# Kernel optimization log

Hardware: AMD Instinct MI355X
Metric: run time of the kernel (lower is better)

The kernel has to match this reference:

```python
import jax, jax.numpy as jnp
import numpy as np

MODES = 256
WIDTH = 64
T_HIST = 1
T_FUT = 1
BATCH = 64
S = 8192


def setup_inputs() -> dict:
    key = jax.random.key(0)
    ks = jax.random.split(key, 12)
    scale = 1.0 / (WIDTH * WIDTH)
    inp = {
        "u": jax.random.normal(ks[0], (BATCH, S, T_HIST), dtype=jnp.float32),
        # lifting layer: Linear(T_HIST+1 -> WIDTH), stored [in, out]
        "fc0_w": jax.random.normal(ks[1], (T_HIST + 1, WIDTH), dtype=jnp.float32) * 0.5,
        "fc0_b": jax.random.normal(ks[2], (WIDTH,), dtype=jnp.float32) * 0.1,
        # 4 spectral conv layers, complex weights stored as real/imag parts
        "sw_r": scale * jax.random.uniform(ks[3], (4, WIDTH, WIDTH, MODES), dtype=jnp.float32),
        "sw_i": scale * jax.random.uniform(ks[4], (4, WIDTH, WIDTH, MODES), dtype=jnp.float32),
        # 4 pointwise (1x1 conv) layers: weight [out,in], bias [out]
        "pw_w": jax.random.normal(ks[5], (4, WIDTH, WIDTH), dtype=jnp.float32) * (1.0 / np.sqrt(WIDTH)),
        "pw_b": jax.random.normal(ks[6], (4, WIDTH), dtype=jnp.float32) * 0.1,
        # projection head
        "fc1_w": jax.random.normal(ks[7], (WIDTH, 128), dtype=jnp.float32) * (1.0 / np.sqrt(WIDTH)),
        "fc1_b": jax.random.normal(ks[8], (128,), dtype=jnp.float32) * 0.1,
        "fc2_w": jax.random.normal(ks[9], (128, T_FUT), dtype=jnp.float32) * (1.0 / np.sqrt(128)),
        "fc2_b": jax.random.normal(ks[10], (T_FUT,), dtype=jnp.float32) * 0.1,
    }
    return inp


def _spectral_conv(x, wr, wi):
    # x: [b, c_in, s] real; weights: [c_in, c_out, MODES] (real/imag parts)
    s = x.shape[-1]
    xf = jnp.fft.rfft(x)                     # [b, c_in, s//2+1] complex
    w = wr + 1j * wi
    om = jnp.einsum('bix,iox->box', xf[:, :, :MODES], w)  # [b, c_out, MODES]
    out_ft = jnp.zeros((x.shape[0], wr.shape[1], s // 2 + 1), dtype=om.dtype)
    out_ft = out_ft.at[:, :, :MODES].set(om)
    return jnp.fft.irfft(out_ft, n=s)        # [b, c_out, s] real


def reference(u, fc0_w, fc0_b, sw_r, sw_i, pw_w, pw_b, fc1_w, fc1_b, fc2_w, fc2_b):
    b, s, _ = u.shape
    grid = jnp.broadcast_to(jnp.linspace(0.0, 1.0, s, dtype=u.dtype)[None, :, None], (b, s, 1))
    x = jnp.concatenate([u, grid], axis=-1)              # [b, s, 2]
    x = x @ fc0_w + fc0_b                                # [b, s, W]
    x = jnp.transpose(x, (0, 2, 1))                      # [b, W, s]
    for l in range(4):
        x1 = _spectral_conv(x, sw_r[l], sw_i[l])
        x2 = jnp.einsum('oi,bis->bos', pw_w[l], x) + pw_b[l][None, :, None]
        x = x1 + x2
        if l < 3:
            x = jax.nn.gelu(x, approximate=False)
    x = jnp.transpose(x, (0, 2, 1))                      # [b, s, W]
    x = jax.nn.gelu(x @ fc1_w + fc1_b, approximate=False)
    x = x @ fc2_w + fc2_b                                # [b, s, T_FUT]
    return x
```

## Files before the change

### kernel.cpp

```cpp
#include <hip/hip_runtime.h>
#include <hip/hip_bf16.h>
#include <math.h>

#define BB 64
#define CC 64
#define SS 8192
#define NMODE 256
#define KK2 512

typedef __attribute__((ext_vector_type(8))) short short8;
typedef __attribute__((ext_vector_type(4))) float f32x4;
typedef __attribute__((ext_vector_type(16))) float f32x16;

__device__ __forceinline__ float gelu_exact(float v) {
    return 0.5f * v * (1.0f + erff(v * 0.7071067811865476f));
}

__device__ __forceinline__ float b2f(ushort u) {
    return __uint_as_float(((unsigned int)u) << 16);
}
__device__ __forceinline__ ushort f2b(float v) {
    __hip_bfloat16 h = __float2bfloat16(v);
    return *(ushort*)&h;
}
__device__ __forceinline__ void split2(float v, ushort& h, ushort& l) {
    h = f2b(v);
    l = f2b(v - b2f(h));
}

__global__ void build_T1(ushort* __restrict__ h, ushort* __restrict__ l) {
    int c = blockIdx.x;
    int n = blockIdx.y * 256 + threadIdx.x;
    int k = c >> 1;
    int m = (n * k) & (SS - 1);
    float th = (float)m * (6.283185307179586476925f / (float)SS);
    float s, co;
    sincosf(th, &s, &co);
    float v = (c & 1) ? -s : co;
    ushort hh, ll;
    split2(v, hh, ll);
    h[(size_t)c * SS + n] = hh;
    l[(size_t)c * SS + n] = ll;
}

__global__ void build_T2(ushort* __restrict__ h, ushort* __restrict__ l) {
    int n = blockIdx.x;
    int c = blockIdx.y * 256 + threadIdx.x;
    int k = c >> 1;
    int m = (n * k) & (SS - 1);
    float th = (float)m * (6.283185307179586476925f / (float)SS);
    float s, co;
    sincosf(th, &s, &co);
    float v = (c & 1) ? -s : co;
    ushort hh, ll;
    split2(v, hh, ll);
    h[(size_t)n * KK2 + c] = hh;
    l[(size_t)n * KK2 + c] = ll;
}

__global__ void zero_xf(float* __restrict__ p) {
    size_t i = ((size_t)blockIdx.x * 256 + threadIdx.x) * 4;
    *(float4*)&p[i] = make_float4(0.f, 0.f, 0.f, 0.f);
}

__global__ void lift_kernel(const float* __restrict__ u, const float* __restrict__ w0,
                            const float* __restrict__ b0, ushort* __restrict__ xh,
                            ushort* __restrict__ xl) {
    int n = blockIdx.x * 256 + threadIdx.x;
    int c = blockIdx.y;
    int b = blockIdx.z;
    float uv = u[b * SS + n];
    float g = (float)n * (1.0f / (float)(SS - 1));
    float v = uv * w0[c] + g * w0[CC + c] + b0[c];
    ushort hh, ll;
    split2(v, hh, ll);
    size_t idx = (size_t)(b * CC + c) * SS + n;
    xh[idx] = hh;
    xl[idx] = ll;
}

__global__ __launch_bounds__(256) void dft_mfma(const ushort* __restrict__ xh,
                                                const ushort* __restrict__ xl,
                                                const ushort* __restrict__ t1h,
                                                const ushort* __restrict__ t1l,
                                                float* __restrict__ Xf) {
    __shared__ __align__(16) ushort SM[16384];
    ushort* As_h = SM;
    ushort* As_l = SM + 4096;
    ushort* Bs_h = SM + 8192;
    ushort* Bs_l = SM + 12288;
    const int t = threadIdx.x;
    const int L = blockIdx.x;
    const int gq = L >> 5, j = L & 31;
    const int c0 = (j >> 3) * 128;
    const int m0 = ((gq & 3) * 8 + (j & 7)) * 128;
    const int kz = (gq >> 2) * (SS / 4);
    const int lane = t & 63, w = t >> 6;
    const int wm = (w >> 1) * 64, wn = (w & 1) * 64;
    const int l32 = lane & 31, lh = lane >> 5;
    const int sr = t >> 1, sh = (t & 1) * 16;
    const int g0 = (t & 1) * 2;
    const int d0 = ((g0 + 0) * 128 + sr) * 8;
    const int d1 = ((g0 + 1) * 128 + sr) * 8;

    f32x16 acc[2][2];
#pragma unroll
    for (int i = 0; i < 2; i++)
#pragma unroll
        for (int jj = 0; jj < 2; jj++) acc[i][jj] = (f32x16)0.f;

    const size_t arow = (size_t)(m0 + sr) * SS;
    const size_t brow = (size_t)(c0 + sr) * SS;
    const int kend = kz + SS / 4;

    short8 a0h, a1h, a0l, a1l, b0h, b1h, b0l, b1l;
    {
        const size_t ga = arow + kz + sh;
        const size_t gb = brow + kz + sh;
        a0h = *(const short8*)&xh[ga];
        a1h = *(const short8*)&xh[ga + 8];
        a0l = *(const short8*)&xl[ga];
        a1l = *(const short8*)&xl[ga + 8];
        b0h = *(const short8*)&t1h[gb];
        b1h = *(const short8*)&t1h[gb + 8];
        b0l = *(const short8*)&t1l[gb];
        b1l = *(const short8*)&t1l[gb + 8];
    }
    for (int kt = kz; kt < kend; kt += 32) {
        __syncthreads();
        *(short8*)&As_h[d0] = a0h;
        *(short8*)&As_h[d1] = a1h;
        *(short8*)&As_l[d0] = a0l;
        *(short8*)&As_l[d1] = a1l;
        *(short8*)&Bs_h[d0] = b0h;
        *(short8*)&Bs_h[d1] = b1h;
        *(short8*)&Bs_l[d0] = b0l;
        *(short8*)&Bs_l[d1] = b1l;
        __syncthreads();
        const int ktn = (kt + 32 < kend) ? kt + 32 : kz;
        const size_t ga = arow + ktn + sh;
        const size_t gb = brow + ktn + sh;
        a0h = *(const short8*)&xh[ga];
        a1h = *(const short8*)&xh[ga + 8];
        a0l = *(const short8*)&xl[ga];
        a1l = *(const short8*)&xl[ga + 8];
        b0h = *(const short8*)&t1h[gb];
        b1h = *(const short8*)&t1h[gb + 8];
        b0l = *(const short8*)&t1l[gb];
        b1l = *(const short8*)&t1l[gb + 8];
#pragma unroll
        for (int s2 = 0; s2 < 2; s2++) {
            const int kg = s2 * 2 + lh;
            short8 ah[2], al[2], bh2[2], bl2[2];
#pragma unroll
            for (int mt = 0; mt < 2; mt++) {
                int off = (kg * 128 + wm + mt * 32 + l32) * 8;
                ah[mt] = *(const short8*)&As_h[off];
                al[mt] = *(const short8*)&As_l[off];
            }
#pragma unroll
            for (int nt = 0; nt < 2; nt++) {
                int off = (kg * 128 + wn + nt * 32 + l32) * 8;
                bh2[nt] = *(const short8*)&Bs_h[off];
                bl2[nt] = *(const short8*)&Bs_l[off];
            }
#pragma unroll
            for (int nt = 0; nt < 2; nt++)
#pragma unroll
                for (int mt = 0; mt < 2; mt++) {
                    acc[mt][nt] = __builtin_amdgcn_mfma_f32_32x32x16_bf16(ah[mt], bh2[nt], acc[mt][nt], 0, 0, 0);
                    acc[mt][nt] = __builtin_amdgcn_mfma_f32_32x32x16_bf16(ah[mt], bl2[nt], acc[mt][nt], 0, 0, 0);
                    acc[mt][nt] = __builtin_amdgcn_mfma_f32_32x32x16_bf16(al[mt], bh2[nt], acc[mt][nt], 0, 0, 0);
                }
        }
    }
#pragma unroll
    for (int mt = 0; mt < 2; mt++)
#pragma unroll
        for (int nt = 0; nt < 2; nt++) {
            int col = c0 + wn + nt * 32 + l32;
#pragma unroll
            for (int reg = 0; reg < 16; reg++) {
                int row = m0 + wm + mt * 32 + (reg & 3) + 8 * (reg >> 2) + 4 * lh;
                atomicAdd(&Xf[(size_t)row * KK2 + col], acc[mt][nt][reg]);
            }
        }
}

__global__ __launch_bounds__(256) void mode_mix(const float* __restrict__ Xf,
                                                const float* __restrict__ swr,
                                                const float* __restrict__ swi,
                                                ushort* __restrict__ omh,
                                                ushort* __restrict__ oml, int l) {
    int k = threadIdx.x;
    int bg = blockIdx.x * 2;
    int og = blockIdx.y * 2;
    float ar[2][2] = {}, ai[2][2] = {};
#pragma unroll 2
    for (int i = 0; i < CC; i++) {
        float2 x0 = *(const float2*)&Xf[((size_t)(bg + 0) * CC + i) * KK2 + 2 * k];
        float2 x1 = *(const float2*)&Xf[((size_t)(bg + 1) * CC + i) * KK2 + 2 * k];
        size_t wb = ((size_t)(l * CC + i) * CC + og) * NMODE + k;
        float wr0 = swr[wb], wi0 = swi[wb];
        float wr1 = swr[wb + NMODE], wi1 = swi[wb + NMODE];
        ar[0][0] += x0.x * wr0 - x0.y * wi0;
        ai[0][0] += x0.x * wi0 + x0.y * wr0;
        ar[0][1] += x0.x * wr1 - x0.y * wi1;
        ai[0][1] += x0.x * wi1 + x0.y * wr1;
        ar[1][0] += x1.x * wr0 - x1.y * wi0;
        ai[1][0] += x1.x * wi0 + x1.y * wr0;
        ar[1][1] += x1.x * wr1 - x1.y * wi1;
        ai[1][1] += x1.x * wi1 + x1.y * wr1;
    }
    float ck = (k == 0) ? (1.0f / (float)SS) : (2.0f / (float)SS);
#pragma unroll
    for (int b2 = 0; b2 < 2; b2++)
#pragma unroll
        for (int oo = 0; oo < 2; oo++) {
            float re = ar[b2][oo] * ck;
            float im = ai[b2][oo] * ck;
            ushort hr, lr2, hi2, li2;
            split2(re, hr, lr2);
            split2(im, hi2, li2);
            size_t base = ((size_t)(bg + b2) * CC + og + oo) * KK2 + 2 * k;
            *(ushort2*)&omh[base] = make_ushort2(hr, hi2);
            *(ushort2*)&oml[base] = make_ushort2(lr2, li2);
        }
}

__global__ __launch_bounds__(256) void inv_mfma(const ushort* __restrict__ omh,
                                                const ushort* __restrict__ oml,
                                                const ushort* __restrict__ t2h,
                                                const ushort* __restrict__ t2l,
                                                const float* __restrict__ pww,
                                                const float* __restrict__ pwb,
                                                ushort* __restrict__ xh,
                                                ushort* __restrict__ xl, int l,
                                                int gel) {
    __shared__ __align__(16) ushort SM[16384];
    ushort* As_h = SM;
    ushort* As_l = SM + 4096;
    ushort* Bs_h = SM + 8192;
    ushort* Bs_l = SM + 12288;
    const int t = threadIdx.x;
    const int n0 = blockIdx.x * 128;
    const int row0 = blockIdx.y * 128;
    const int lane = t & 63, w = t >> 6;
    const int wm = (w >> 1) * 64, wn = (w & 1) * 64;
    const int l32 = lane & 31, lh = lane >> 5;
    const int sr = t >> 1, sh = (t & 1) * 16;
    const int g0 = (t & 1) * 2;
    const int d0 = ((g0 + 0) * 128 + sr) * 8;
    const int d1 = ((g0 + 1) * 128 + sr) * 8;
    const int xrowb = row0 + wm;

    short8 pk_h[2][2], pk_l[2][2];
#pragma unroll
    for (int nt = 0; nt < 2; nt++) {
        int ncol = n0 + wn + nt * 32 + l32;
#pragma unroll
        for (int s2 = 0; s2 < 2; s2++)
#pragma unroll
            for (int jj = 0; jj < 8; jj++) {
                size_t gxi = (size_t)(xrowb + s2 * 16 + lh * 8 + jj) * SS + ncol;
                pk_h[nt][s2][jj] = (short)xh[gxi];
                pk_l[nt][s2][jj] = (short)xl[gxi];
            }
    }

    f32x16 acc[2][2];
#pragma unroll
    for (int i = 0; i < 2; i++)
#pragma unroll
        for (int jj = 0; jj < 2; jj++) acc[i][jj] = (f32x16)0.f;

    const size_t arow = (size_t)(row0 + sr) * KK2;
    const size_t brow = (size_t)(n0 + sr) * KK2;

    short8 a0h, a1h, a0l, a1l, b0h, b1h, b0l, b1l;
    {
        const size_t ga = arow + sh;
        const size_t gb = brow + sh;
        a0h = *(const short8*)&omh[ga];
        a1h = *(const short8*)&omh[ga + 8];
        a0l = *(const short8*)&oml[ga];
        a1l = *(const short8*)&oml[ga + 8];
        b0h = *(const short8*)&t2h[gb];
        b1h = *(const short8*)&t2h[gb + 8];
        b0l = *(const short8*)&t2l[gb];
        b1l = *(const short8*)&t2l[gb + 8];
    }
    for (int kt = 0; kt < KK2; kt += 32) {
        __syncthreads();
        *(short8*)&As_h[d0] = a0h;
        *(short8*)&As_h[d1] = a1h;
        *(short8*)&As_l[d0] = a0l;
        *(short8*)&As_l[d1] = a1l;
        *(short8*)&Bs_h[d0] = b0h;
        *(short8*)&Bs_h[d1] = b1h;
        *(short8*)&Bs_l[d0] = b0l;
        *(short8*)&Bs_l[d1] = b1l;
        __syncthreads();
        const int ktn = (kt + 32 < KK2) ? kt + 32 : 0;
        const size_t ga = arow + ktn + sh;
        const size_t gb = brow + ktn + sh;
        a0h = *(const short8*)&omh[ga];
        a1h = *(const short8*)&omh[ga + 8];
        a0l = *(const short8*)&oml[ga];
        a1l = *(const short8*)&oml[ga + 8];
        b0h = *(const short8*)&t2h[gb];
        b1h = *(const short8*)&t2h[gb + 8];
        b0l = *(const short8*)&t2l[gb];
        b1l = *(const short8*)&t2l[gb + 8];
#pragma unroll
        for (int s2 = 0; s2 < 2; s2++) {
            const int kg = s2 * 2 + lh;
            short8 ah[2], al[2], bh2[2], bl2[2];
#pragma unroll
            for (int mt = 0; mt < 2; mt++) {
                int off = (kg * 128 + wm + mt * 32 + l32) * 8;
                ah[mt] = *(const short8*)&As_h[off];
                al[mt] = *(const short8*)&As_l[off];
            }
#pragma unroll
            for (int nt = 0; nt < 2; nt++) {
                int off = (kg * 128 + wn + nt * 32 + l32) * 8;
                bh2[nt] = *(const short8*)&Bs_h[off];
                bl2[nt] = *(const short8*)&Bs_l[off];
            }
#pragma unroll
            for (int nt = 0; nt < 2; nt++)
#pragma unroll
                for (int mt = 0; mt < 2; mt++) {
                    acc[mt][nt] = __builtin_amdgcn_mfma_f32_32x32x16_bf16(ah[mt], bh2[nt], acc[mt][nt], 0, 0, 0);
                    acc[mt][nt] = __builtin_amdgcn_mfma_f32_32x32x16_bf16(ah[mt], bl2[nt], acc[mt][nt], 0, 0, 0);
                    acc[mt][nt] = __builtin_amdgcn_mfma_f32_32x32x16_bf16(al[mt], bh2[nt], acc[mt][nt], 0, 0, 0);
                }
        }
    }
    short8 s1h[2][2], s1l[2][2];
#pragma unroll
    for (int nt = 0; nt < 2; nt++) {
        int ncol = n0 + wn + nt * 32 + l32;
#pragma unroll
        for (int s2 = 0; s2 < 2; s2++)
#pragma unroll
            for (int jj = 0; jj < 8; jj++) {
                size_t gxi = (size_t)(xrowb + 32 + s2 * 16 + lh * 8 + jj) * SS + ncol;
                s1h[nt][s2][jj] = (short)xh[gxi];
                s1l[nt][s2][jj] = (short)xl[gxi];
            }
    }
#pragma unroll
    for (int s = 0; s < 2; s++) {
#pragma unroll
        for (int s2 = 0; s2 < 2; s2++) {
            short8 pah[2], pal[2];
#pragma unroll
            for (int mt = 0; mt < 2; mt++) {
                int o = mt * 32 + l32;
                const float* pp = &pww[(size_t)(l * CC + o) * CC + s * 32 + s2 * 16 + lh * 8];
                float4 pa = *(const float4*)pp;
                float4 pb = *(const float4*)(pp + 4);
                float pv[8] = {pa.x, pa.y, pa.z, pa.w, pb.x, pb.y, pb.z, pb.w};
#pragma unroll
                for (int e = 0; e < 8; e++) {
                    ushort h2, l2;
                    split2(pv[e], h2, l2);
                    pah[mt][e] = (short)h2;
                    pal[mt][e] = (short)l2;
                }
            }
#pragma unroll
            for (int nt = 0; nt < 2; nt++) {
                short8 bh = s ? s1h[nt][s2] : pk_h[nt][s2];
                short8 bl = s ? s1l[nt][s2] : pk_l[nt][s2];
#pragma unroll
                for (int mt = 0; mt < 2; mt++) {
                    acc[mt][nt] = __builtin_amdgcn_mfma_f32_32x32x16_bf16(pah[mt], bh, acc[mt][nt], 0, 0, 0);
                    acc[mt][nt] = __builtin_amdgcn_mfma_f32_32x32x16_bf16(pah[mt], bl, acc[mt][nt], 0, 0, 0);
                    acc[mt][nt] = __builtin_amdgcn_mfma_f32_32x32x16_bf16(pal[mt], bh, acc[mt][nt], 0, 0, 0);
                }
            }
        }
    }
#pragma unroll
    for (int mt = 0; mt < 2; mt++)
#pragma unroll
        for (int reg = 0; reg < 16; reg++) {
            int roffs = (reg & 3) + 8 * (reg >> 2) + 4 * lh;
            int o = mt * 32 + roffs;
            float bias = pwb[l * CC + o];
            size_t rowg = (size_t)(row0 + wm + o) * SS;
#pragma unroll
            for (int nt = 0; nt < 2; nt++) {
                int n = n0 + wn + nt * 32 + l32;
                float v = acc[mt][nt][reg] + bias;
                if (gel) v = gelu_exact(v);
                ushort h2, l2;
                split2(v, h2, l2);
                xh[rowg + n] = h2;
                xl[rowg + n] = l2;
            }
        }
}

__global__ __launch_bounds__(256) void head_kernel(const ushort* __restrict__ xh,
                                                   const ushort* __restrict__ xl,
                                                   const float* __restrict__ w1,
                                                   const float* __restrict__ b1,
                                                   const float* __restrict__ w2,
                                                   const float* __restrict__ b2,
                                                   float* __restrict__ out) {
    __shared__ float Xs[64][64];
    __shared__ float W1s[64][128];
    __shared__ float part[4][64];
    int b = blockIdx.y;
    int n0 = blockIdx.x * 64;
    int tid = threadIdx.x;
    {
        int c = tid >> 2, nq = tid & 3;
        size_t gx = (size_t)(b * CC + c) * SS + n0 + nq * 16;
        short8 hA = *(const short8*)&xh[gx];
        short8 hB = *(const short8*)&xh[gx + 8];
        short8 lA = *(const short8*)&xl[gx];
        short8 lB = *(const short8*)&xl[gx + 8];
#pragma unroll
        for (int e = 0; e < 8; e++) {
            Xs[c][nq * 16 + e] = b2f((ushort)hA[e]) + b2f((ushort)lA[e]);
            Xs[c][nq * 16 + 8 + e] = b2f((ushort)hB[e]) + b2f((ushort)lB[e]);
        }
    }
    float* w1flat = &W1s[0][0];
#pragma unroll
    for (int q = 0; q < 8; q++) {
        int off = q * 1024 + tid * 4;
        *(float4*)&w1flat[off] = *(const float4*)&w1[off];
    }
    __syncthreads();
    int nn = tid & 63, jg = tid >> 6;
    float h[32];
#pragma unroll
    for (int jj = 0; jj < 32; jj++) h[jj] = b1[jg * 32 + jj];
    for (int c = 0; c < 64; c++) {
        float xv = Xs[c][nn];
#pragma unroll
        for (int jj = 0; jj < 32; jj++)
            h[jj] = fmaf(xv, W1s[c][jg * 32 + jj], h[jj]);
    }
    float p = 0.f;
#pragma unroll
    for (int jj = 0; jj < 32; jj++)
        p = fmaf(gelu_exact(h[jj]), w2[jg * 32 + jj], p);
    part[jg][nn] = p;
    __syncthreads();
    if (tid < 64) {
        float v = part[0][tid] + part[1][tid] + part[2][tid] + part[3][tid] + b2[0];
        out[b * SS + n0 + tid] = v;
    }
}

extern "C" void kernel_launch(void* const* d_in, const int* in_sizes, int n_in,
                              void* d_out, int out_size, void* d_ws, size_t ws_size,
                              hipStream_t stream) {
    (void)in_sizes; (void)n_in; (void)out_size; (void)ws_size;
    const float* u = (const float*)d_in[0];
    const float* fc0_w = (const float*)d_in[1];
    const float* fc0_b = (const float*)d_in[2];
    const float* sw_r = (const float*)d_in[3];
    const float* sw_i = (const float*)d_in[4];
    const float* pw_w = (const float*)d_in[5];
    const float* pw_b = (const float*)d_in[6];
    const float* fc1_w = (const float*)d_in[7];
    const float* fc1_b = (const float*)d_in[8];
    const float* fc2_w = (const float*)d_in[9];
    const float* fc2_b = (const float*)d_in[10];
    float* out = (float*)d_out;

    char* ws = (char*)d_ws;
    ushort* xh = (ushort*)ws;
    ushort* xl = (ushort*)(ws + 67108864);
    ushort* t1h = (ushort*)(ws + 134217728);
    ushort* t1l = (ushort*)(ws + 142606336);
    ushort* t2h = (ushort*)(ws + 150994944);
    ushort* t2l = (ushort*)(ws + 159383552);
    ushort* omh = (ushort*)(ws + 167772160);
    ushort* oml = (ushort*)(ws + 171966464);
    float* Xf = (float*)(ws + 176160768);

    build_T1<<<dim3(KK2, SS / 256), 256, 0, stream>>>(t1h, t1l);
    build_T2<<<dim3(SS, KK2 / 256), 256, 0, stream>>>(t2h, t2l);
    lift_kernel<<<dim3(SS / 256, CC, BB), 256, 0, stream>>>(u, fc0_w, fc0_b, xh, xl);

    for (int l = 0; l < 4; l++) {
        zero_xf<<<dim3(2048), 256, 0, stream>>>(Xf);
        dft_mfma<<<dim3(512), 256, 0, stream>>>(xh, xl, t1h, t1l, Xf);
        mode_mix<<<dim3(BB / 2, CC / 2), 256, 0, stream>>>(Xf, sw_r, sw_i, omh, oml, l);
        inv_mfma<<<dim3(SS / 128, BB / 2), 256, 0, stream>>>(
            omh, oml, t2h, t2l, pw_w, pw_b, xh, xl, l, (l < 3) ? 1 : 0);
    }
    head_kernel<<<dim3(SS / 64, BB), 256, 0, stream>>>(xh, xl, fc1_w, fc1_b, fc2_w,
                                                       fc2_b, out);
}
```

Before: 1.579 ms.

## Double-buffer LDS tiles in DFT and inverse MFMA GEMM loops

```diff
diff --git a/kernel.cpp b/kernel.cpp
--- a/kernel.cpp
+++ b/kernel.cpp
@@ -9,7 +9,6 @@
 #define KK2 512
 
 typedef __attribute__((ext_vector_type(8))) short short8;
-typedef __attribute__((ext_vector_type(4))) float f32x4;
 typedef __attribute__((ext_vector_type(16))) float f32x16;
 
 __device__ __forceinline__ float gelu_exact(float v) {
@@ -84,11 +83,11 @@
                                                 const ushort* __restrict__ t1h,
                                                 const ushort* __restrict__ t1l,
                                                 float* __restrict__ Xf) {
-    __shared__ __align__(16) ushort SM[16384];
+    __shared__ __align__(16) ushort SM[32768];
     ushort* As_h = SM;
-    ushort* As_l = SM + 4096;
-    ushort* Bs_h = SM + 8192;
-    ushort* Bs_l = SM + 12288;
+    ushort* As_l = SM + 8192;
+    ushort* Bs_h = SM + 16384;
+    ushort* Bs_l = SM + 24576;
     const int t = threadIdx.x;
     const int L = blockIdx.x;
     const int gq = L >> 5, j = L & 31;
@@ -111,7 +110,7 @@
 
     const size_t arow = (size_t)(m0 + sr) * SS;
     const size_t brow = (size_t)(c0 + sr) * SS;
-    const int kend = kz + SS / 4;
+    const int NS = (SS / 4) / 32;
 
     short8 a0h, a1h, a0l, a1l, b0h, b1h, b0l, b1l;
     {
@@ -126,18 +125,19 @@
         b0l = *(const short8*)&t1l[gb];
         b1l = *(const short8*)&t1l[gb + 8];
     }
-    for (int kt = kz; kt < kend; kt += 32) {
-        __syncthreads();
-        *(short8*)&As_h[d0] = a0h;
-        *(short8*)&As_h[d1] = a1h;
-        *(short8*)&As_l[d0] = a0l;
-        *(short8*)&As_l[d1] = a1l;
-        *(short8*)&Bs_h[d0] = b0h;
-        *(short8*)&Bs_h[d1] = b1h;
-        *(short8*)&Bs_l[d0] = b0l;
-        *(short8*)&Bs_l[d1] = b1l;
-        __syncthreads();
-        const int ktn = (kt + 32 < kend) ? kt + 32 : kz;
+    *(short8*)&As_h[d0] = a0h;
+    *(short8*)&As_h[d1] = a1h;
+    *(short8*)&As_l[d0] = a0l;
+    *(short8*)&As_l[d1] = a1l;
+    *(short8*)&Bs_h[d0] = b0h;
+    *(short8*)&Bs_h[d1] = b1h;
+    *(short8*)&Bs_l[d0] = b0l;
+    *(short8*)&Bs_l[d1] = b1l;
+    __syncthreads();
+
+    for (int hs = 0; hs < NS; hs++) {
+        const int cur = (hs & 1) * 4096, nxt = cur ^ 4096;
+        const int ktn = kz + ((hs + 1 < NS) ? (hs + 1) * 32 : 0);
         const size_t ga = arow + ktn + sh;
         const size_t gb = brow + ktn + sh;
         a0h = *(const short8*)&xh[ga];
@@ -154,13 +154,13 @@
             short8 ah[2], al[2], bh2[2], bl2[2];
 #pragma unroll
             for (int mt = 0; mt < 2; mt++) {
-                int off = (kg * 128 + wm + mt * 32 + l32) * 8;
+                int off = cur + (kg * 128 + wm + mt * 32 + l32) * 8;
                 ah[mt] = *(const short8*)&As_h[off];
                 al[mt] = *(const short8*)&As_l[off];
             }
 #pragma unroll
             for (int nt = 0; nt < 2; nt++) {
-                int off = (kg * 128 + wn + nt * 32 + l32) * 8;
+                int off = cur + (kg * 128 + wn + nt * 32 + l32) * 8;
                 bh2[nt] = *(const short8*)&Bs_h[off];
                 bl2[nt] = *(const short8*)&Bs_l[off];
             }
@@ -173,6 +173,15 @@
                     acc[mt][nt] = __builtin_amdgcn_mfma_f32_32x32x16_bf16(al[mt], bh2[nt], acc[mt][nt], 0, 0, 0);
                 }
         }
+        *(short8*)&As_h[nxt + d0] = a0h;
+        *(short8*)&As_h[nxt + d1] = a1h;
+        *(short8*)&As_l[nxt + d0] = a0l;
+        *(short8*)&As_l[nxt + d1] = a1l;
+        *(short8*)&Bs_h[nxt + d0] = b0h;
+        *(short8*)&Bs_h[nxt + d1] = b1h;
+        *(short8*)&Bs_l[nxt + d0] = b0l;
+        *(short8*)&Bs_l[nxt + d1] = b1l;
+        __syncthreads();
     }
 #pragma unroll
     for (int mt = 0; mt < 2; mt++)
@@ -237,11 +246,11 @@
                                                 ushort* __restrict__ xh,
                                                 ushort* __restrict__ xl, int l,
                                                 int gel) {
-    __shared__ __align__(16) ushort SM[16384];
+    __shared__ __align__(16) ushort SM[32768];
     ushort* As_h = SM;
-    ushort* As_l = SM + 4096;
-    ushort* Bs_h = SM + 8192;
-    ushort* Bs_l = SM + 12288;
+    ushort* As_l = SM + 8192;
+    ushort* Bs_h = SM + 16384;
+    ushort* Bs_l = SM + 24576;
     const int t = threadIdx.x;
     const int n0 = blockIdx.x * 128;
     const int row0 = blockIdx.y * 128;
@@ -276,6 +285,7 @@
 
     const size_t arow = (size_t)(row0 + sr) * KK2;
     const size_t brow = (size_t)(n0 + sr) * KK2;
+    const int NS = KK2 / 32;
 
     short8 a0h, a1h, a0l, a1l, b0h, b1h, b0l, b1l;
     {
@@ -290,18 +300,19 @@
         b0l = *(const short8*)&t2l[gb];
         b1l = *(const short8*)&t2l[gb + 8];
     }
-    for (int kt = 0; kt < KK2; kt += 32) {
-        __syncthreads();
-        *(short8*)&As_h[d0] = a0h;
-        *(short8*)&As_h[d1] = a1h;
-        *(short8*)&As_l[d0] = a0l;
-        *(short8*)&As_l[d1] = a1l;
-        *(short8*)&Bs_h[d0] = b0h;
-        *(short8*)&Bs_h[d1] = b1h;
-        *(short8*)&Bs_l[d0] = b0l;
-        *(short8*)&Bs_l[d1] = b1l;
-        __syncthreads();
-        const int ktn = (kt + 32 < KK2) ? kt + 32 : 0;
+    *(short8*)&As_h[d0] = a0h;
+    *(short8*)&As_h[d1] = a1h;
+    *(short8*)&As_l[d0] = a0l;
+    *(short8*)&As_l[d1] = a1l;
+    *(short8*)&Bs_h[d0] = b0h;
+    *(short8*)&Bs_h[d1] = b1h;
+    *(short8*)&Bs_l[d0] = b0l;
+    *(short8*)&Bs_l[d1] = b1l;
+    __syncthreads();
+
+    for (int hs = 0; hs < NS; hs++) {
+        const int cur = (hs & 1) * 4096, nxt = cur ^ 4096;
+        const int ktn = (hs + 1 < NS) ? (hs + 1) * 32 : 0;
         const size_t ga = arow + ktn + sh;
         const size_t gb = brow + ktn + sh;
         a0h = *(const short8*)&omh[ga];
@@ -318,13 +329,13 @@
             short8 ah[2], al[2], bh2[2], bl2[2];
 #pragma unroll
             for (int mt = 0; mt < 2; mt++) {
-                int off = (kg * 128 + wm + mt * 32 + l32) * 8;
+                int off = cur + (kg * 128 + wm + mt * 32 + l32) * 8;
                 ah[mt] = *(const short8*)&As_h[off];
                 al[mt] = *(const short8*)&As_l[off];
             }
 #pragma unroll
             for (int nt = 0; nt < 2; nt++) {
-                int off = (kg * 128 + wn + nt * 32 + l32) * 8;
+                int off = cur + (kg * 128 + wn + nt * 32 + l32) * 8;
                 bh2[nt] = *(const short8*)&Bs_h[off];
                 bl2[nt] = *(const short8*)&Bs_l[off];
             }
@@ -337,6 +348,15 @@
                     acc[mt][nt] = __builtin_amdgcn_mfma_f32_32x32x16_bf16(al[mt], bh2[nt], acc[mt][nt], 0, 0, 0);
                 }
         }
+        *(short8*)&As_h[nxt + d0] = a0h;
+        *(short8*)&As_h[nxt + d1] = a1h;
+        *(short8*)&As_l[nxt + d0] = a0l;
+        *(short8*)&As_l[nxt + d1] = a1l;
+        *(short8*)&Bs_h[nxt + d0] = b0h;
+        *(short8*)&Bs_h[nxt + d1] = b1h;
+        *(short8*)&Bs_l[nxt + d0] = b0l;
+        *(short8*)&Bs_l[nxt + d1] = b1l;
+        __syncthreads();
     }
     short8 s1h[2][2], s1l[2][2];
 #pragma unroll
```

New measurement: 1.590 ms. Within noise of the previous version (+0.7%).

## Split DFT reduction 8-way, stage pointwise input through LDS, add occupancy hints

Applied to the files above, without the earlier changes.

```diff
diff --git a/kernel.cpp b/kernel.cpp
--- a/kernel.cpp
+++ b/kernel.cpp
@@ -9,7 +9,6 @@
 #define KK2 512
 
 typedef __attribute__((ext_vector_type(8))) short short8;
-typedef __attribute__((ext_vector_type(4))) float f32x4;
 typedef __attribute__((ext_vector_type(16))) float f32x16;
 
 __device__ __forceinline__ float gelu_exact(float v) {
@@ -79,11 +78,11 @@
     xl[idx] = ll;
 }
 
-__global__ __launch_bounds__(256) void dft_mfma(const ushort* __restrict__ xh,
-                                                const ushort* __restrict__ xl,
-                                                const ushort* __restrict__ t1h,
-                                                const ushort* __restrict__ t1l,
-                                                float* __restrict__ Xf) {
+__global__ __launch_bounds__(256, 3) void dft_mfma(const ushort* __restrict__ xh,
+                                                   const ushort* __restrict__ xl,
+                                                   const ushort* __restrict__ t1h,
+                                                   const ushort* __restrict__ t1l,
+                                                   float* __restrict__ Xf) {
     __shared__ __align__(16) ushort SM[16384];
     ushort* As_h = SM;
     ushort* As_l = SM + 4096;
@@ -94,7 +93,7 @@
     const int gq = L >> 5, j = L & 31;
     const int c0 = (j >> 3) * 128;
     const int m0 = ((gq & 3) * 8 + (j & 7)) * 128;
-    const int kz = (gq >> 2) * (SS / 4);
+    const int kz = (gq >> 2) * (SS / 8);
     const int lane = t & 63, w = t >> 6;
     const int wm = (w >> 1) * 64, wn = (w & 1) * 64;
     const int l32 = lane & 31, lh = lane >> 5;
@@ -111,7 +110,7 @@
 
     const size_t arow = (size_t)(m0 + sr) * SS;
     const size_t brow = (size_t)(c0 + sr) * SS;
-    const int kend = kz + SS / 4;
+    const int kend = kz + SS / 8;
 
     short8 a0h, a1h, a0l, a1l, b0h, b1h, b0l, b1l;
     {
@@ -228,16 +227,16 @@
         }
 }
 
-__global__ __launch_bounds__(256) void inv_mfma(const ushort* __restrict__ omh,
-                                                const ushort* __restrict__ oml,
-                                                const ushort* __restrict__ t2h,
-                                                const ushort* __restrict__ t2l,
-                                                const float* __restrict__ pww,
-                                                const float* __restrict__ pwb,
-                                                ushort* __restrict__ xh,
-                                                ushort* __restrict__ xl, int l,
-                                                int gel) {
-    __shared__ __align__(16) ushort SM[16384];
+__global__ __launch_bounds__(256, 3) void inv_mfma(const ushort* __restrict__ omh,
+                                                   const ushort* __restrict__ oml,
+                                                   const ushort* __restrict__ t2h,
+                                                   const ushort* __restrict__ t2l,
+                                                   const float* __restrict__ pww,
+                                                   const float* __restrict__ pwb,
+                                                   ushort* __restrict__ xh,
+                                                   ushort* __restrict__ xl, int l,
+                                                   int gel) {
+    __shared__ __align__(16) ushort SM[17408];
     ushort* As_h = SM;
     ushort* As_l = SM + 4096;
     ushort* Bs_h = SM + 8192;
@@ -252,21 +251,6 @@
     const int g0 = (t & 1) * 2;
     const int d0 = ((g0 + 0) * 128 + sr) * 8;
     const int d1 = ((g0 + 1) * 128 + sr) * 8;
-    const int xrowb = row0 + wm;
-
-    short8 pk_h[2][2], pk_l[2][2];
-#pragma unroll
-    for (int nt = 0; nt < 2; nt++) {
-        int ncol = n0 + wn + nt * 32 + l32;
-#pragma unroll
-        for (int s2 = 0; s2 < 2; s2++)
-#pragma unroll
-            for (int jj = 0; jj < 8; jj++) {
-                size_t gxi = (size_t)(xrowb + s2 * 16 + lh * 8 + jj) * SS + ncol;
-                pk_h[nt][s2][jj] = (short)xh[gxi];
-                pk_l[nt][s2][jj] = (short)xl[gxi];
-            }
-    }
 
     f32x16 acc[2][2];
 #pragma unroll
@@ -338,28 +322,26 @@
                 }
         }
     }
-    short8 s1h[2][2], s1l[2][2];
-#pragma unroll
-    for (int nt = 0; nt < 2; nt++) {
-        int ncol = n0 + wn + nt * 32 + l32;
-#pragma unroll
-        for (int s2 = 0; s2 < 2; s2++)
-#pragma unroll
-            for (int jj = 0; jj < 8; jj++) {
-                size_t gxi = (size_t)(xrowb + 32 + s2 * 16 + lh * 8 + jj) * SS + ncol;
-                s1h[nt][s2][jj] = (short)xh[gxi];
-                s1l[nt][s2][jj] = (short)xl[gxi];
-            }
-    }
+    ushort* Xs = SM;
+    const int xr = t >> 1, xc = (t & 1) * 64;
+    const size_t xg = (size_t)(row0 + xr) * SS + n0 + xc;
 #pragma unroll
     for (int s = 0; s < 2; s++) {
-#pragma unroll
-        for (int s2 = 0; s2 < 2; s2++) {
+        const ushort* src = s ? xl : xh;
+        short8 v[8];
+#pragma unroll
+        for (int q = 0; q < 8; q++) v[q] = *(const short8*)&src[xg + q * 8];
+        __syncthreads();
+#pragma unroll
+        for (int q = 0; q < 8; q++) *(short8*)&Xs[xr * 136 + xc + q * 8] = v[q];
+        __syncthreads();
+#pragma unroll
+        for (int ks = 0; ks < 4; ks++) {
             short8 pah[2], pal[2];
 #pragma unroll
             for (int mt = 0; mt < 2; mt++) {
                 int o = mt * 32 + l32;
-                const float* pp = &pww[(size_t)(l * CC + o) * CC + s * 32 + s2 * 16 + lh * 8];
+                const float* pp = &pww[(size_t)(l * CC + o) * CC + ks * 16 + lh * 8];
                 float4 pa = *(const float4*)pp;
                 float4 pb = *(const float4*)(pp + 4);
                 float pv[8] = {pa.x, pa.y, pa.z, pa.w, pb.x, pb.y, pb.z, pb.w};
@@ -373,13 +355,15 @@
             }
 #pragma unroll
             for (int nt = 0; nt < 2; nt++) {
-                short8 bh = s ? s1h[nt][s2] : pk_h[nt][s2];
-                short8 bl = s ? s1l[nt][s2] : pk_l[nt][s2];
+                short8 bf;
+                const int rbase = (wm + ks * 16 + lh * 8) * 136 + wn + nt * 32 + l32;
+#pragma unroll
+                for (int jj = 0; jj < 8; jj++) bf[jj] = (short)Xs[rbase + jj * 136];
 #pragma unroll
                 for (int mt = 0; mt < 2; mt++) {
-                    acc[mt][nt] = __builtin_amdgcn_mfma_f32_32x32x16_bf16(pah[mt], bh, acc[mt][nt], 0, 0, 0);
-                    acc[mt][nt] = __builtin_amdgcn_mfma_f32_32x32x16_bf16(pah[mt], bl, acc[mt][nt], 0, 0, 0);
-                    acc[mt][nt] = __builtin_amdgcn_mfma_f32_32x32x16_bf16(pal[mt], bh, acc[mt][nt], 0, 0, 0);
+                    acc[mt][nt] = __builtin_amdgcn_mfma_f32_32x32x16_bf16(pah[mt], bf, acc[mt][nt], 0, 0, 0);
+                    if (s == 0)
+                        acc[mt][nt] = __builtin_amdgcn_mfma_f32_32x32x16_bf16(pal[mt], bf, acc[mt][nt], 0, 0, 0);
                 }
             }
         }
@@ -494,7 +478,7 @@
 
     for (int l = 0; l < 4; l++) {
         zero_xf<<<dim3(2048), 256, 0, stream>>>(Xf);
-        dft_mfma<<<dim3(512), 256, 0, stream>>>(xh, xl, t1h, t1l, Xf);
+        dft_mfma<<<dim3(1024), 256, 0, stream>>>(xh, xl, t1h, t1l, Xf);
         mode_mix<<<dim3(BB / 2, CC / 2), 256, 0, stream>>>(Xf, sw_r, sw_i, omh, oml, l);
         inv_mfma<<<dim3(SS / 128, BB / 2), 256, 0, stream>>>(
             omh, oml, t2h, t2l, pw_w, pw_b, xh, xl, l, (l < 3) ? 1 : 0);
```

Result: slower. 1.720 ms (+9.0%).
